# Kernel optimization log

Measured on AMD Instinct MI355X. Metric: run time of the kernel, lower is better.

## Reference

```python
import jax, jax.numpy as jnp
import numpy as np

B, S, F = 8, 2048, 1024
NEG = -1000000000.0

def setup_inputs() -> dict:
    key = jax.random.key(0)
    ks = jax.random.split(key, 8)
    x = jax.random.normal(ks[0], (B, S, F), dtype=jnp.float32)
    # causal attention mask [S, S], 1 = keep, 0 = masked
    attn_mask = jnp.tril(jnp.ones((S, S), dtype=jnp.int32))
    # key padding mask [B, 1, S], random 0/1
    pad_mask = jax.random.randint(ks[1], (B, 1, S), 0, 2, dtype=jnp.int32)
    # ensure at least the first key position is valid per batch to avoid all-masked rows
    pad_mask = pad_mask.at[:, :, 0].set(1)
    sc = 1.0 / np.sqrt(F).astype(np.float32)
    Wq = jax.random.normal(ks[2], (F, F), dtype=jnp.float32) * sc
    bq = jax.random.normal(ks[3], (F,), dtype=jnp.float32) * 0.01
    Wk = jax.random.normal(ks[4], (F, F), dtype=jnp.float32) * sc
    bk = jax.random.normal(ks[5], (F,), dtype=jnp.float32) * 0.01
    Wv = jax.random.normal(ks[6], (F, F), dtype=jnp.float32) * sc
    bv = jax.random.normal(ks[7], (F,), dtype=jnp.float32) * 0.01
    return {"x": x, "attn_mask": attn_mask, "pad_mask": pad_mask,
            "Wq": Wq, "bq": bq, "Wk": Wk, "bk": bk, "Wv": Wv, "bv": bv}

def reference(x, attn_mask, pad_mask, Wq, bq, Wk, bk, Wv, bv):
    # torch Linear: y = x @ W.T + b
    q = jnp.einsum('bsf,of->bso', x, Wq) + bq
    k = jnp.einsum('bsf,of->bso', x, Wk) + bk
    v = jnp.einsum('bsf,of->bso', x, Wv) + bv
    scale = 1.0 / jnp.sqrt(jnp.asarray(q.shape[-1], dtype=x.dtype))
    scores = jnp.einsum('bqf,bkf->bqk', q, k) * scale  # [B, S, S]
    scores = jnp.where(pad_mask == 0, NEG, scores)            # pad_mask [B,1,S] broadcasts
    scores = jnp.where(attn_mask[None, :, :] == 0, NEG, scores)
    prob = jax.nn.softmax(scores, axis=-1)
    # dropout=0.0 (eval / identity)
    return jnp.einsum('bqk,bkf->bqf', prob, v)
```

## Files before the change

### kernel.cpp

```cpp
#include <hip/hip_runtime.h>
#include <hip/hip_bf16.h>
#include <stdint.h>


#define S_LEN 2048
#define F_DIM 1024
#define NBATCH 8
#define BS_TOT (NBATCH * S_LEN)

typedef __attribute__((ext_vector_type(8))) short bf16x8;
typedef __attribute__((ext_vector_type(4))) float f32x4;
typedef unsigned short u16;

__device__ __forceinline__ u16 f32_to_bf16_rne(float f) {
    union { float f; uint32_t u; } v; v.f = f;
    uint32_t u = v.u;
    u += 0x7FFFu + ((u >> 16) & 1u);
    return (u16)(u >> 16);
}
__device__ __forceinline__ float bf16_to_f32(u16 h) {
    union { uint32_t u; float f; } v; v.u = ((uint32_t)h) << 16;
    return v.f;
}

__device__ __forceinline__ void gload_lds16(const u16* g, u16* l) {
    __builtin_amdgcn_global_load_lds(
        (const __attribute__((address_space(1))) void*)g,
        (__attribute__((address_space(3))) void*)l,
        16, 0, 0);
}

__global__ __launch_bounds__(256) void cvt_f32_bf16(const float* __restrict__ in,
                                                    u16* __restrict__ out, int n) {
    int i = (blockIdx.x * 256 + threadIdx.x) * 4;
    if (i + 3 < n) {
        float4 f = *(const float4*)(in + i);
        ushort4 o;
        o.x = f32_to_bf16_rne(f.x); o.y = f32_to_bf16_rne(f.y);
        o.z = f32_to_bf16_rne(f.z); o.w = f32_to_bf16_rne(f.w);
        *(ushort4*)(out + i) = o;
    }
}

__global__ __launch_bounds__(256) void cvt_w3(const float* __restrict__ Wq,
                                              const float* __restrict__ Wk,
                                              const float* __restrict__ Wv,
                                              u16* __restrict__ Wb) {
    const int which = blockIdx.y;
    const float* in = (which == 0) ? Wq : (which == 1) ? Wk : Wv;
    int i = (blockIdx.x * 256 + threadIdx.x) * 4;
    float4 f = *(const float4*)(in + i);
    ushort4 o;
    o.x = f32_to_bf16_rne(f.x); o.y = f32_to_bf16_rne(f.y);
    o.z = f32_to_bf16_rne(f.z); o.w = f32_to_bf16_rne(f.w);
    *(ushort4*)(Wb + (size_t)which * F_DIM * F_DIM + i) = o;
}

template<class Epi>
__device__ __forceinline__ void gemm_tile_128(
    const u16* __restrict__ A, int lda,
    const u16* __restrict__ Bt, int ldb,
    int m0, int n0, int K, float alpha, Epi epi)
{
    __shared__ u16 la[128 * 32];
    __shared__ u16 lb[128 * 32];

    const int tid  = threadIdx.x;
    const int lane = tid & 63;
    const int wave = tid >> 6;
    const int wm = (wave & 1) * 64;
    const int wn = (wave >> 1) * 64;

    f32x4 acc[4][4];
#pragma unroll
    for (int mt = 0; mt < 4; mt++)
#pragma unroll
        for (int nt = 0; nt < 4; nt++)
            acc[mt][nt] = f32x4{0.f, 0.f, 0.f, 0.f};

    const int mrow = wm + (lane & 15);
    const int nrow = wn + (lane & 15);
    const int koff = (lane >> 4) * 8;

    const int cb0 = wave * 64;
    const int cb1 = wave * 64 + 256;
    const int lrow = lane >> 2;
    const int lcol = (lane & 3) * 8;
    const u16* pa0 = A  + (size_t)(m0 + (cb0 >> 2) + lrow) * lda + lcol;
    const u16* pa1 = A  + (size_t)(m0 + (cb1 >> 2) + lrow) * lda + lcol;
    const u16* pb0 = Bt + (size_t)(n0 + (cb0 >> 2) + lrow) * ldb + lcol;
    const u16* pb1 = Bt + (size_t)(n0 + (cb1 >> 2) + lrow) * ldb + lcol;
    u16* qa0 = la + cb0 * 8;
    u16* qa1 = la + cb1 * 8;
    u16* qb0 = lb + cb0 * 8;
    u16* qb1 = lb + cb1 * 8;

    for (int kk = 0; kk < K; kk += 32) {
        __syncthreads();
        gload_lds16(pa0 + kk, qa0);
        gload_lds16(pa1 + kk, qa1);
        gload_lds16(pb0 + kk, qb0);
        gload_lds16(pb1 + kk, qb1);
        __syncthreads();

        bf16x8 fa[4], fb[4];
#pragma unroll
        for (int t = 0; t < 4; t++) {
            fa[t] = *(const bf16x8*)(la + (mrow + t * 16) * 32 + koff);
            fb[t] = *(const bf16x8*)(lb + (nrow + t * 16) * 32 + koff);
        }
#pragma unroll
        for (int mt = 0; mt < 4; mt++)
#pragma unroll
            for (int nt = 0; nt < 4; nt++)
                acc[mt][nt] = __builtin_amdgcn_mfma_f32_16x16x32_bf16(
                    fa[mt], fb[nt], acc[mt][nt], 0, 0, 0);
    }

    const int col   = lane & 15;
    const int rquad = (lane >> 4) * 4;
#pragma unroll
    for (int mt = 0; mt < 4; mt++)
#pragma unroll
        for (int nt = 0; nt < 4; nt++) {
            const int n = n0 + wn + nt * 16 + col;
#pragma unroll
            for (int r = 0; r < 4; r++) {
                const int m = m0 + wm + mt * 16 + rquad + r;
                epi(m, n, acc[mt][nt][r] * alpha);
            }
        }
}

__global__ __launch_bounds__(256) void k_qkv(const u16* __restrict__ xb,
                                             const u16* __restrict__ Wb,
                                             const float* __restrict__ bq,
                                             const float* __restrict__ bk,
                                             const float* __restrict__ bv,
                                             u16* __restrict__ q,
                                             u16* __restrict__ k,
                                             u16* __restrict__ vT) {
    const int which = blockIdx.y;
    const int bx = blockIdx.x;
    const int xcd = bx & 7;
    const int idx = bx >> 3;
    const int m0 = (xcd * 16 + (idx >> 3)) * 128;
    const int n0 = (idx & 7) * 128;
    const float* bias = (which == 0) ? bq : (which == 1) ? bk : bv;
    const u16* W = Wb + (size_t)which * F_DIM * F_DIM;
    if (which < 2) {
        u16* o = (which == 0) ? q : k;
        gemm_tile_128(xb, F_DIM, W, F_DIM, m0, n0, F_DIM, 1.0f,
            [&](int m, int n, float v) {
                o[(size_t)m * F_DIM + n] = f32_to_bf16_rne(v + bias[n]);
            });
    } else {
        gemm_tile_128(xb, F_DIM, W, F_DIM, m0, n0, F_DIM, 1.0f,
            [&](int m, int n, float v) {
                vT[((size_t)(m >> 11) * F_DIM + n) * S_LEN + (m & 2047)] =
                    f32_to_bf16_rne(v + bias[n]);
            });
    }
}

__global__ __launch_bounds__(256) void k_scores(const u16* __restrict__ q,
                                                const u16* __restrict__ k,
                                                const int* __restrict__ pad,
                                                u16* __restrict__ Pp) {
    const int b = blockIdx.x & 7;
    const int t = blockIdx.x >> 3;
    int it = 0, base = 0;
    while (base + it + 1 <= t) { base += it + 1; it++; }
    const int jt = t - base;
    const int* padb = pad + b * S_LEN;
    u16* Pb = Pp + (size_t)b * S_LEN * S_LEN;
    gemm_tile_128(q + (size_t)b * S_LEN * F_DIM, F_DIM,
                  k + (size_t)b * S_LEN * F_DIM, F_DIM,
                  it * 128, jt * 128, F_DIM, 0.03125f,
        [&](int m, int n, float v) {
            u16 o = 0;
            if (n <= m && padb[n] != 0)
                o = f32_to_bf16_rne(__expf(v - 16.0f));
            Pb[(size_t)m * S_LEN + n] = o;
        });
}

__global__ __launch_bounds__(256) void k_rowsum(const u16* __restrict__ Pp,
                                                float* __restrict__ invl) {
    const int wave = threadIdx.x >> 6, lane = threadIdx.x & 63;
    const int r = blockIdx.x * 4 + wave;
    const int b = r >> 11, i = r & 2047;
    const int jlim = ((i >> 7) + 1) << 7;
    const u16* row = Pp + (size_t)b * S_LEN * S_LEN + (size_t)i * S_LEN;
    float s = 0.f;
    for (int j0 = lane * 8; j0 < jlim; j0 += 512) {
        bf16x8 v = *(const bf16x8*)(row + j0);
#pragma unroll
        for (int e = 0; e < 8; e++) s += bf16_to_f32((u16)v[e]);
    }
    for (int off = 32; off > 0; off >>= 1) s += __shfl_xor(s, off);
    if (lane == 0) invl[r] = 1.0f / s;
}

__global__ __launch_bounds__(256) void k_pv(const u16* __restrict__ Pp,
                                            const u16* __restrict__ vT,
                                            const float* __restrict__ invl,
                                            float* __restrict__ out) {
    const int b = blockIdx.x & 7;
    const int rest = blockIdx.x >> 3;
    const int it = rest >> 3;
    const int nt = rest & 7;
    const int Keff = (it + 1) * 128;
    const float* il = invl + b * S_LEN;
    float* ob = out + (size_t)b * S_LEN * F_DIM;
    gemm_tile_128(Pp + (size_t)b * S_LEN * S_LEN, S_LEN,
                  vT + (size_t)b * F_DIM * S_LEN, S_LEN,
                  it * 128, nt * 128, Keff, 1.0f,
        [&](int m, int n, float v) {
            ob[(size_t)m * F_DIM + n] = v * il[m];
        });
}

extern "C" void kernel_launch(void* const* d_in, const int* in_sizes, int n_in,
                              void* d_out, int out_size, void* d_ws, size_t ws_size,
                              hipStream_t stream) {
    const float* x  = (const float*)d_in[0];
    const int* pad  = (const int*)d_in[2];
    const float* Wq = (const float*)d_in[3];
    const float* bq = (const float*)d_in[4];
    const float* Wk = (const float*)d_in[5];
    const float* bk = (const float*)d_in[6];
    const float* Wv = (const float*)d_in[7];
    const float* bv = (const float*)d_in[8];
    float* out = (float*)d_out;

    char* ws = (char*)d_ws;
    u16* q    = (u16*)(ws);
    u16* k    = (u16*)(ws + 32ull * 1024 * 1024);
    u16* vT   = (u16*)(ws + 64ull * 1024 * 1024);
    u16* Pp   = (u16*)(ws + 96ull * 1024 * 1024);
    u16* xb   = (u16*)(ws + 160ull * 1024 * 1024);
    u16* Wb   = (u16*)(ws + 192ull * 1024 * 1024);
    float* il = (float*)(ws + 200ull * 1024 * 1024);

    const int BSF = BS_TOT * F_DIM;
    const int FF = F_DIM * F_DIM;

    cvt_f32_bf16<<<BSF / 1024, 256, 0, stream>>>(x, xb, BSF);
    cvt_w3<<<dim3(FF / 1024, 3), 256, 0, stream>>>(Wq, Wk, Wv, Wb);

    k_qkv<<<dim3(1024, 3), 256, 0, stream>>>(xb, Wb, bq, bk, bv, q, k, vT);

    k_scores<<<1088, 256, 0, stream>>>(q, k, pad, Pp);

    k_rowsum<<<4096, 256, 0, stream>>>(Pp, il);

    k_pv<<<1024, 256, 0, stream>>>(Pp, vT, il, out);
}
```

Baseline: 402.1 us.

## Use 256x256 tiled, 8-wave pipelined GEMM for QKV projection

Replaces the 128x128 tile GEMM in the QKV projection with a new 256x256 tile kernel run by 512 threads. It uses double-buffered, XOR-swizzled LDS staging with interleaved async global-to-LDS loads, split phases separated by barriers, and s_setprio around the MFMA bursts. Larger tiles raise arithmetic intensity and cut redundant global loads of x and W, and the pipelining aims to hide load latency. The grid drops to 768 blocks, and the kernel needs much more LDS and registers per block (8x4 accumulators), which may reduce occupancy.

```diff
diff --git a/kernel.cpp b/kernel.cpp
--- a/kernel.cpp
+++ b/kernel.cpp
@@ -132,7 +132,157 @@
         }
 }
 
-__global__ __launch_bounds__(256) void k_qkv(const u16* __restrict__ xb,
+__device__ __forceinline__ bf16x8 lds_frag(const u16* plane, int row, int g) {
+    const char* p = (const char*)plane + row * 64 + ((g ^ ((row >> 1) & 3)) << 4);
+    return *(const bf16x8*)p;
+}
+
+template<class Epi>
+__device__ __forceinline__ void gemm_tile_256(
+    const u16* __restrict__ A, int lda,
+    const u16* __restrict__ Bt, int ldb,
+    int m0, int n0, int K, float alpha, Epi epi)
+{
+    __shared__ u16 lds[2][2][2][8192];
+
+    const int tid  = threadIdx.x;
+    const int lane = tid & 63;
+    const int wave = tid >> 6;
+    const int wm   = (wave >> 2) * 128;
+    const int wn   = (wave & 3) * 64;
+    const int frow = lane & 15;
+    const int g    = lane >> 4;
+    const int wvo  = wave * 512;
+
+    f32x4 acc[8][4];
+#pragma unroll
+    for (int i = 0; i < 8; i++)
+#pragma unroll
+        for (int j = 0; j < 4; j++) acc[i][j] = f32x4{0.f, 0.f, 0.f, 0.f};
+
+    const int gG = (tid & 3) ^ ((tid >> 3) & 3);
+    const u16* pa0 = A  + (size_t)(m0 + (tid >> 2)) * lda + gG * 8;
+    const u16* pa1 = pa0 + (size_t)128 * lda;
+    const u16* pb0 = Bt + (size_t)(n0 + (tid >> 2)) * ldb + gG * 8;
+    const u16* pb1 = pb0 + (size_t)128 * ldb;
+
+    auto stageA = [&](int kc, u16* slot) {
+        gload_lds16(pa0 + kc, slot + wvo);
+        gload_lds16(pa1 + kc, slot + 4096 + wvo);
+    };
+    auto stageB = [&](int kc, u16* slot) {
+        gload_lds16(pb0 + kc, slot + wvo);
+        gload_lds16(pb1 + kc, slot + 4096 + wvo);
+    };
+
+    const int nk = K >> 6;
+
+    stageA(0,  &lds[0][0][0][0]);
+    stageB(0,  &lds[0][1][0][0]);
+    stageA(32, &lds[0][0][1][0]);
+    stageB(32, &lds[0][1][1][0]);
+    stageA(64, &lds[1][0][0][0]);
+    stageB(64, &lds[1][1][0][0]);
+    asm volatile("s_waitcnt vmcnt(8)" ::: "memory");
+    asm volatile("s_barrier" ::: "memory");
+
+    for (int t = 0; t < nk; ++t) {
+        const int buf = t & 1;
+        const u16* Ap0 = &lds[buf][0][0][0];
+        const u16* Ap1 = &lds[buf][0][1][0];
+        const u16* Bp0 = &lds[buf][1][0][0];
+        const u16* Bp1 = &lds[buf][1][1][0];
+        u16* nA1 = &lds[buf ^ 1][0][1][0];
+        u16* nB1 = &lds[buf ^ 1][1][1][0];
+        u16* nA0 = &lds[buf][0][0][0];
+        u16* nB0 = &lds[buf][1][0][0];
+        const bool ep = (t >= nk - 2);
+        const int kc1 = ((t + 1) << 6);
+        const int kc2 = ((t + 2) << 6);
+
+        bf16x8 fa[4], fb[4];
+
+#pragma unroll
+        for (int mt = 0; mt < 4; mt++) fa[mt] = lds_frag(Ap0, wm + mt * 16 + frow, g);
+#pragma unroll
+        for (int nt = 0; nt < 4; nt++) fb[nt] = lds_frag(Bp0, wn + nt * 16 + frow, g);
+        if (t + 1 < nk) stageA(kc1 + 32, nA1);
+        asm volatile("s_barrier" ::: "memory");
+        __builtin_amdgcn_s_setprio(1);
+#pragma unroll
+        for (int mt = 0; mt < 4; mt++)
+#pragma unroll
+            for (int nt = 0; nt < 4; nt++)
+                acc[mt][nt] = __builtin_amdgcn_mfma_f32_16x16x32_bf16(
+                    fa[mt], fb[nt], acc[mt][nt], 0, 0, 0);
+        __builtin_amdgcn_s_setprio(0);
+        asm volatile("s_barrier" ::: "memory");
+
+#pragma unroll
+        for (int mt = 0; mt < 4; mt++) fa[mt] = lds_frag(Ap0, wm + 64 + mt * 16 + frow, g);
+        if (t + 1 < nk) stageB(kc1 + 32, nB1);
+        if (ep) asm volatile("s_waitcnt vmcnt(0)" ::: "memory");
+        else    asm volatile("s_waitcnt vmcnt(8)" ::: "memory");
+        asm volatile("s_barrier" ::: "memory");
+        __builtin_amdgcn_s_setprio(1);
+#pragma unroll
+        for (int mt = 0; mt < 4; mt++)
+#pragma unroll
+            for (int nt = 0; nt < 4; nt++)
+                acc[4 + mt][nt] = __builtin_amdgcn_mfma_f32_16x16x32_bf16(
+                    fa[mt], fb[nt], acc[4 + mt][nt], 0, 0, 0);
+        __builtin_amdgcn_s_setprio(0);
+        asm volatile("s_barrier" ::: "memory");
+
+#pragma unroll
+        for (int mt = 0; mt < 4; mt++) fa[mt] = lds_frag(Ap1, wm + mt * 16 + frow, g);
+#pragma unroll
+        for (int nt = 0; nt < 4; nt++) fb[nt] = lds_frag(Bp1, wn + nt * 16 + frow, g);
+        if (t + 2 < nk) stageA(kc2, nA0);
+        asm volatile("s_barrier" ::: "memory");
+        __builtin_amdgcn_s_setprio(1);
+#pragma unroll
+        for (int mt = 0; mt < 4; mt++)
+#pragma unroll
+            for (int nt = 0; nt < 4; nt++)
+                acc[mt][nt] = __builtin_amdgcn_mfma_f32_16x16x32_bf16(
+                    fa[mt], fb[nt], acc[mt][nt], 0, 0, 0);
+        __builtin_amdgcn_s_setprio(0);
+        asm volatile("s_barrier" ::: "memory");
+
+#pragma unroll
+        for (int mt = 0; mt < 4; mt++) fa[mt] = lds_frag(Ap1, wm + 64 + mt * 16 + frow, g);
+        if (t + 2 < nk) stageB(kc2, nB0);
+        if (ep) asm volatile("s_waitcnt vmcnt(0)" ::: "memory");
+        else    asm volatile("s_waitcnt vmcnt(8)" ::: "memory");
+        asm volatile("s_barrier" ::: "memory");
+        __builtin_amdgcn_s_setprio(1);
+#pragma unroll
+        for (int mt = 0; mt < 4; mt++)
+#pragma unroll
+            for (int nt = 0; nt < 4; nt++)
+                acc[4 + mt][nt] = __builtin_amdgcn_mfma_f32_16x16x32_bf16(
+                    fa[mt], fb[nt], acc[4 + mt][nt], 0, 0, 0);
+        __builtin_amdgcn_s_setprio(0);
+        asm volatile("s_barrier" ::: "memory");
+    }
+
+    const int col   = lane & 15;
+    const int rquad = (lane >> 4) * 4;
+#pragma unroll
+    for (int mt = 0; mt < 8; mt++)
+#pragma unroll
+        for (int nt = 0; nt < 4; nt++) {
+            const int n = n0 + wn + nt * 16 + col;
+#pragma unroll
+            for (int r = 0; r < 4; r++) {
+                const int m = m0 + wm + mt * 16 + rquad + r;
+                epi(m, n, acc[mt][nt][r] * alpha);
+            }
+        }
+}
+
+__global__ __launch_bounds__(512) void k_qkv(const u16* __restrict__ xb,
                                              const u16* __restrict__ Wb,
                                              const float* __restrict__ bq,
                                              const float* __restrict__ bk,
@@ -144,23 +294,20 @@
     const int bx = blockIdx.x;
     const int xcd = bx & 7;
     const int idx = bx >> 3;
-    const int m0 = (xcd * 16 + (idx >> 3)) * 128;
-    const int n0 = (idx & 7) * 128;
+    const int m0 = (xcd * 8 + (idx >> 2)) * 256;
+    const int n0 = (idx & 3) * 256;
     const float* bias = (which == 0) ? bq : (which == 1) ? bk : bv;
     const u16* W = Wb + (size_t)which * F_DIM * F_DIM;
-    if (which < 2) {
-        u16* o = (which == 0) ? q : k;
-        gemm_tile_128(xb, F_DIM, W, F_DIM, m0, n0, F_DIM, 1.0f,
-            [&](int m, int n, float v) {
-                o[(size_t)m * F_DIM + n] = f32_to_bf16_rne(v + bias[n]);
-            });
-    } else {
-        gemm_tile_128(xb, F_DIM, W, F_DIM, m0, n0, F_DIM, 1.0f,
-            [&](int m, int n, float v) {
-                vT[((size_t)(m >> 11) * F_DIM + n) * S_LEN + (m & 2047)] =
-                    f32_to_bf16_rne(v + bias[n]);
-            });
-    }
+    u16* o = (which == 0) ? q : k;
+    gemm_tile_256(xb, F_DIM, W, F_DIM, m0, n0, F_DIM, 1.0f,
+        [&](int m, int n, float v) {
+            u16 val = f32_to_bf16_rne(v + bias[n]);
+            if (which < 2) {
+                o[(size_t)m * F_DIM + n] = val;
+            } else {
+                vT[((size_t)(m >> 11) * F_DIM + n) * S_LEN + (m & 2047)] = val;
+            }
+        });
 }
 
 __global__ __launch_bounds__(256) void k_scores(const u16* __restrict__ q,
@@ -249,7 +396,7 @@
     cvt_f32_bf16<<<BSF / 1024, 256, 0, stream>>>(x, xb, BSF);
     cvt_w3<<<dim3(FF / 1024, 3), 256, 0, stream>>>(Wq, Wk, Wv, Wb);
 
-    k_qkv<<<dim3(1024, 3), 256, 0, stream>>>(xb, Wb, bq, bk, bv, q, k, vT);
+    k_qkv<<<dim3(256, 3), 512, 0, stream>>>(xb, Wb, bq, bk, bv, q, k, vT);
 
     k_scores<<<1088, 256, 0, stream>>>(q, k, pad, Pp);
 
```

Measured after the change: 415.9 us. 3.4% more time.

## Fuse softmax row-sum into scores kernel via atomics and balance PV tile order

Applied to the files above, without the earlier changes.

The separate row-sum kernel is removed. Each scores tile now accumulates per-row partial sums of the bf16 probabilities in registers, reduces them with wave shuffles, and atomically adds them into a zeroed buffer. The PV kernel takes reciprocals of these sums up front and interleaves large and small causal row tiles so the uneven work is spread better across blocks. This removes a full re-read of the probability matrix at the cost of a memset, atomics, and added register pressure in the scores epilogue. It also relies on the lambda's (m,n) to register mapping matching the assumed MFMA layout.

```diff
diff --git a/kernel.cpp b/kernel.cpp
--- a/kernel.cpp
+++ b/kernel.cpp
@@ -166,7 +166,8 @@
 __global__ __launch_bounds__(256) void k_scores(const u16* __restrict__ q,
                                                 const u16* __restrict__ k,
                                                 const int* __restrict__ pad,
-                                                u16* __restrict__ Pp) {
+                                                u16* __restrict__ Pp,
+                                                float* __restrict__ lsum) {
     const int b = blockIdx.x & 7;
     const int t = blockIdx.x >> 3;
     int it = 0, base = 0;
@@ -174,6 +175,11 @@
     const int jt = t - base;
     const int* padb = pad + b * S_LEN;
     u16* Pb = Pp + (size_t)b * S_LEN * S_LEN;
+
+    float rs[16];
+#pragma unroll
+    for (int i = 0; i < 16; i++) rs[i] = 0.f;
+
     gemm_tile_128(q + (size_t)b * S_LEN * F_DIM, F_DIM,
                   k + (size_t)b * S_LEN * F_DIM, F_DIM,
                   it * 128, jt * 128, F_DIM, 0.03125f,
@@ -182,42 +188,56 @@
             if (n <= m && padb[n] != 0)
                 o = f32_to_bf16_rne(__expf(v - 16.0f));
             Pb[(size_t)m * S_LEN + n] = o;
+            const int i = m & 63;
+            rs[((i >> 4) << 2) | (i & 3)] += bf16_to_f32(o);
         });
-}
-
-__global__ __launch_bounds__(256) void k_rowsum(const u16* __restrict__ Pp,
-                                                float* __restrict__ invl) {
-    const int wave = threadIdx.x >> 6, lane = threadIdx.x & 63;
-    const int r = blockIdx.x * 4 + wave;
-    const int b = r >> 11, i = r & 2047;
-    const int jlim = ((i >> 7) + 1) << 7;
-    const u16* row = Pp + (size_t)b * S_LEN * S_LEN + (size_t)i * S_LEN;
-    float s = 0.f;
-    for (int j0 = lane * 8; j0 < jlim; j0 += 512) {
-        bf16x8 v = *(const bf16x8*)(row + j0);
-#pragma unroll
-        for (int e = 0; e < 8; e++) s += bf16_to_f32((u16)v[e]);
-    }
-    for (int off = 32; off > 0; off >>= 1) s += __shfl_xor(s, off);
-    if (lane == 0) invl[r] = 1.0f / s;
+
+    const int lane  = threadIdx.x & 63;
+    const int wave  = threadIdx.x >> 6;
+    const int wm    = (wave & 1) * 64;
+    const int rquad = (lane >> 4) * 4;
+    float* lb = lsum + b * S_LEN + it * 128 + wm;
+#pragma unroll
+    for (int i = 0; i < 16; i++) {
+        float s = rs[i];
+        s += __shfl_xor(s, 1);
+        s += __shfl_xor(s, 2);
+        s += __shfl_xor(s, 4);
+        s += __shfl_xor(s, 8);
+        if ((lane & 15) == 0)
+            atomicAdd(&lb[((i >> 2) << 4) + rquad + (i & 3)], s);
+    }
 }
 
 __global__ __launch_bounds__(256) void k_pv(const u16* __restrict__ Pp,
                                             const u16* __restrict__ vT,
-                                            const float* __restrict__ invl,
+                                            const float* __restrict__ lsum,
                                             float* __restrict__ out) {
     const int b = blockIdx.x & 7;
     const int rest = blockIdx.x >> 3;
-    const int it = rest >> 3;
+    const int j = rest >> 3;
     const int nt = rest & 7;
+    const int it = (j & 1) ? (j >> 1) : (15 - (j >> 1));
     const int Keff = (it + 1) * 128;
-    const float* il = invl + b * S_LEN;
+    const float* ls = lsum + b * S_LEN;
     float* ob = out + (size_t)b * S_LEN * F_DIM;
+
+    const int lane  = threadIdx.x & 63;
+    const int wave  = threadIdx.x >> 6;
+    const int wm    = (wave & 1) * 64;
+    const int rquad = (lane >> 4) * 4;
+    const int mb    = it * 128 + wm;
+    float myinv[16];
+#pragma unroll
+    for (int i = 0; i < 16; i++)
+        myinv[i] = 1.0f / ls[mb + ((i >> 2) << 4) + rquad + (i & 3)];
+
     gemm_tile_128(Pp + (size_t)b * S_LEN * S_LEN, S_LEN,
                   vT + (size_t)b * F_DIM * S_LEN, S_LEN,
                   it * 128, nt * 128, Keff, 1.0f,
         [&](int m, int n, float v) {
-            ob[(size_t)m * F_DIM + n] = v * il[m];
+            const int i = m & 63;
+            ob[(size_t)m * F_DIM + n] = v * myinv[((i >> 4) << 2) | (i & 3)];
         });
 }
 
@@ -246,14 +266,14 @@
     const int BSF = BS_TOT * F_DIM;
     const int FF = F_DIM * F_DIM;
 
+    hipMemsetAsync(il, 0, BS_TOT * sizeof(float), stream);
+
     cvt_f32_bf16<<<BSF / 1024, 256, 0, stream>>>(x, xb, BSF);
     cvt_w3<<<dim3(FF / 1024, 3), 256, 0, stream>>>(Wq, Wk, Wv, Wb);
 
     k_qkv<<<dim3(1024, 3), 256, 0, stream>>>(xb, Wb, bq, bk, bv, q, k, vT);
 
-    k_scores<<<1088, 256, 0, stream>>>(q, k, pad, Pp);
-
-    k_rowsum<<<4096, 256, 0, stream>>>(Pp, il);
+    k_scores<<<1088, 256, 0, stream>>>(q, k, pad, Pp, il);
 
     k_pv<<<1024, 256, 0, stream>>>(Pp, vT, il, out);
 }
```

Result: no change. 407.0 us (+1.2%).
